# Kernel tuning notes

Measured on AMD Instinct MI355X. Metric: run time of the kernel, lower is better.

The kernel has to match this reference:

```python
import jax, jax.numpy as jnp
import numpy as np

B, N, K, H, HEADS = 4, 2000, 30, 128, 4
D = H // HEADS  # per-head dim = 32
NUM_IN = 2 * H
NEG_INF = jnp.float32(np.finfo(np.float32).min)


def setup_inputs() -> dict:
    key = jax.random.key(0)
    ks = jax.random.split(key, 10)
    h_V = jax.random.normal(ks[0], (B, N, H), jnp.float32)
    h_EV = jax.random.normal(ks[1], (B, N, K, NUM_IN), jnp.float32)
    h_KV = jax.random.normal(ks[2], (B, N, K, H), jnp.float32)
    h_KE = jax.random.normal(ks[3], (B, N, K, H), jnp.float32)
    mask_attend = (jax.random.uniform(ks[4], (B, N, K)) > 0.2).astype(jnp.float32)
    s = 1.0 / np.sqrt(H)
    W_Q = jax.random.normal(ks[5], (H, H), jnp.float32) * s
    W_K1 = jax.random.normal(ks[6], (H, H), jnp.float32) * s
    W_K2 = jax.random.normal(ks[7], (H, H), jnp.float32) * s
    W_V = jax.random.normal(ks[8], (H, NUM_IN), jnp.float32) * (1.0 / np.sqrt(NUM_IN))
    W_O = jax.random.normal(ks[9], (H, H), jnp.float32) * s
    return {"h_V": h_V, "h_EV": h_EV, "h_KV": h_KV, "h_KE": h_KE,
            "mask_attend": mask_attend, "W_Q": W_Q, "W_K1": W_K1,
            "W_K2": W_K2, "W_V": W_V, "W_O": W_O}


def reference(h_V, h_EV, h_KV, h_KE, mask_attend, W_Q, W_K1, W_K2, W_V, W_O):
    # Projections (torch Linear: y = x @ W.T)
    Q = (h_V @ W_Q.T).reshape(B, N, 1, HEADS, D)          # broadcast over K
    K1 = (h_KE @ W_K1.T).reshape(B, N, K, HEADS, D)
    K2 = (h_KV @ W_K2.T).reshape(B, N, K, HEADS, D)
    V = (h_EV @ W_V.T).reshape(B, N, K, HEADS, D)
    # Trilinear score: sum_d Q*K1*K2 -> [B,N,K,h] -> [B,N,h,K], scaled by 1/d
    logits = jnp.einsum('bnkhd,bnkhd->bnkh', Q * K1, K2)
    logits = jnp.transpose(logits, (0, 1, 3, 2)) / D      # [B,N,h,K]
    # Masked softmax over neighbor axis
    mask = jnp.broadcast_to(mask_attend[:, :, None, :], logits.shape)
    logits = jnp.where(mask > 0, logits, NEG_INF)
    attend = jax.nn.softmax(logits, axis=-1) * mask       # [B,N,h,K]
    # Weighted aggregation over neighbors
    h_upd = jnp.einsum('bnhk,bnkhd->bnhd', attend, V).reshape(B, N, H)
    return h_upd @ W_O.T
```

## Files before the change

kernel.cpp:

```cpp
#include <hip/hip_runtime.h>


#define KNB 30
#define HH 128
#define NUMIN 256
#define TOK 8000
#define TOTROW (TOK*KNB)
#define TB 2
#define NBLK (TOK/TB)
#define SAW 136

typedef __bf16 bf16x8 __attribute__((ext_vector_type(8)));
typedef __bf16 bf16x4_t __attribute__((ext_vector_type(4)));
typedef float f32x4 __attribute__((ext_vector_type(4)));

__global__ __launch_bounds__(256) void conv_w_kernel(
    const float* __restrict__ wk1, const float* __restrict__ wk2,
    const float* __restrict__ wv, __bf16* __restrict__ ws) {
  int e = (blockIdx.x * 256 + threadIdx.x) * 4;
  const float* src; int off;
  if (e < 16384)      { src = wk1; off = e; }
  else if (e < 32768) { src = wk2; off = e - 16384; }
  else                { src = wv;  off = e - 32768; }
  float4 v = *(const float4*)(src + off);
  bf16x4_t o4;
  o4.x = (__bf16)v.x; o4.y = (__bf16)v.y; o4.z = (__bf16)v.z; o4.w = (__bf16)v.w;
  *(bf16x4_t*)(ws + e) = o4;
}

__global__ __launch_bounds__(256, 4) void na_main_kernel(
    const float* __restrict__ h_V, const float* __restrict__ h_EV,
    const float* __restrict__ h_KV, const float* __restrict__ h_KE,
    const float* __restrict__ maskp, const float* __restrict__ W_Q,
    const float* __restrict__ W_O, const __bf16* __restrict__ bW,
    float* __restrict__ out) {
  __shared__ __bf16 sA[2][64 * SAW];
  __shared__ float sQ[TB][HH];
  __shared__ float sU[TB][HH];
  __shared__ float sMask[TB][32];

  const int tid = threadIdx.x;
  const int lane = tid & 63;
  const int wave = tid >> 6;
  const int m = lane & 15;
  const int quad = lane >> 4;
  const int t0 = blockIdx.x * TB;

  const __bf16* bWK1 = bW;
  const __bf16* bWK2 = bW + 16384;
  const __bf16* bWV  = bW + 32768;

  const int srow = tid >> 5;
  const int scol = (tid & 31) << 2;
  float4 sv[8];
  const long r0 = (long)t0 * KNB + srow;

  auto stage_load = [&](const float* base, int ld, int coloff) {
#pragma unroll
    for (int j = 0; j < 8; j++) {
      long rr = r0 + j * 8;
      if (rr > TOTROW - 1) rr = TOTROW - 1;
      sv[j] = *(const float4*)(base + rr * ld + coloff + scol);
    }
  };
  auto stage_store = [&](int b) {
#pragma unroll
    for (int j = 0; j < 8; j++) {
      bf16x4_t o;
      o.x = (__bf16)sv[j].x; o.y = (__bf16)sv[j].y;
      o.z = (__bf16)sv[j].z; o.w = (__bf16)sv[j].w;
      *(bf16x4_t*)&sA[b][(srow + j * 8) * SAW + scol] = o;
    }
  };

  f32x4 accA[4][2], accB[4][2];
  const f32x4 fzero = {0.f, 0.f, 0.f, 0.f};
  auto gemm = [&](const __bf16* gW, int ldw, int kb, const __bf16* Ab,
                  f32x4 (*acc)[2]) {
#pragma unroll
    for (int ks = 0; ks < 4; ks++) {
      const int kc = kb + ks * 32 + quad * 8;
      bf16x8 b0 = *(const bf16x8*)(gW + (wave * 32 + m) * ldw + kc);
      bf16x8 b1 = *(const bf16x8*)(gW + (wave * 32 + 16 + m) * ldw + kc);
#pragma unroll
      for (int mt = 0; mt < 4; mt++) {
        bf16x8 a = *(const bf16x8*)&Ab[(mt * 16 + m) * SAW + ks * 32 + quad * 8];
        acc[mt][0] = __builtin_amdgcn_mfma_f32_16x16x32_bf16(a, b0, acc[mt][0], 0, 0, 0);
        acc[mt][1] = __builtin_amdgcn_mfma_f32_16x16x32_bf16(a, b1, acc[mt][1], 0, 0, 0);
      }
    }
  };

  stage_load(h_KE, HH, 0);
  if (tid < TB * KNB)
    sMask[tid / KNB][tid % KNB] = maskp[(long)t0 * KNB + tid];
  {
    const int t = tid >> 7, o = tid & 127;
    const float4* wq = (const float4*)(W_Q + o * HH);
    const float4* hv = (const float4*)(h_V + (long)(t0 + t) * HH);
    float acc = 0.f;
#pragma unroll
    for (int j = 0; j < 32; j++) {
      float4 a = hv[j], b = wq[j];
      acc += a.x * b.x + a.y * b.y + a.z * b.z + a.w * b.w;
    }
    sQ[t][o] = acc;
  }
  stage_store(0);
  __syncthreads();

  stage_load(h_KV, HH, 0);
#pragma unroll
  for (int mt = 0; mt < 4; mt++) { accA[mt][0] = fzero; accA[mt][1] = fzero; }
  gemm(bWK1, HH, 0, sA[0], accA);
  stage_store(1);
  __syncthreads();

#pragma unroll
  for (int mt = 0; mt < 4; mt++) { accB[mt][0] = fzero; accB[mt][1] = fzero; }
  gemm(bWK2, HH, 0, sA[1], accB);
#pragma unroll
  for (int mt = 0; mt < 4; mt++) {
    accA[mt][0] *= accB[mt][0];
    accA[mt][1] *= accB[mt][1];
  }

  stage_load(h_EV, NUMIN, 0);

  float q0[2], q1[2];
#pragma unroll
  for (int nt = 0; nt < 2; nt++) {
    q0[nt] = sQ[0][wave * 32 + nt * 16 + m];
    q1[nt] = sQ[1][wave * 32 + nt * 16 + m];
  }
  float lg[4][4];
#pragma unroll
  for (int mt = 0; mt < 4; mt++)
#pragma unroll
    for (int r = 0; r < 4; r++) {
      int R = mt * 16 + quad * 4 + r;
      float qa0 = (R < 30) ? q0[0] : q1[0];
      float qa1 = (R < 30) ? q0[1] : q1[1];
      lg[mt][r] = accA[mt][0][r] * qa0 + accA[mt][1][r] * qa1;
    }
#pragma unroll
  for (int d = 1; d < 16; d <<= 1)
#pragma unroll
    for (int mt = 0; mt < 4; mt++)
#pragma unroll
      for (int r = 0; r < 4; r++)
        lg[mt][r] += __shfl_xor(lg[mt][r], d);

  float mx0 = -3.0e38f, mx1 = -3.0e38f;
#pragma unroll
  for (int mt = 0; mt < 4; mt++)
#pragma unroll
    for (int r = 0; r < 4; r++) {
      int R = mt * 16 + quad * 4 + r;
      if (R < 60) {
        int t = R >= 30, k = R - 30 * t;
        float l = (sMask[t][k] > 0.f) ? lg[mt][r] * 0.03125f : -3.0e38f;
        lg[mt][r] = l;
        if (t == 0) mx0 = fmaxf(mx0, l); else mx1 = fmaxf(mx1, l);
      } else lg[mt][r] = -3.0e38f;
    }
  mx0 = fmaxf(mx0, __shfl_xor(mx0, 16)); mx0 = fmaxf(mx0, __shfl_xor(mx0, 32));
  mx1 = fmaxf(mx1, __shfl_xor(mx1, 16)); mx1 = fmaxf(mx1, __shfl_xor(mx1, 32));
  float s0 = 0.f, s1 = 0.f;
  float at[4][4];
#pragma unroll
  for (int mt = 0; mt < 4; mt++)
#pragma unroll
    for (int r = 0; r < 4; r++) {
      int R = mt * 16 + quad * 4 + r;
      float e = 0.f;
      if (R < 60) {
        int t = R >= 30, k = R - 30 * t;
        if (sMask[t][k] > 0.f) {
          float mxt = (t == 0) ? mx0 : mx1;
          e = __expf(lg[mt][r] - mxt);
        }
        if (t == 0) s0 += e; else s1 += e;
      }
      at[mt][r] = e;
    }
  s0 += __shfl_xor(s0, 16); s0 += __shfl_xor(s0, 32);
  s1 += __shfl_xor(s1, 16); s1 += __shfl_xor(s1, 32);
  float inv0 = (s0 > 0.f) ? 1.f / s0 : 0.f;
  float inv1 = (s1 > 0.f) ? 1.f / s1 : 0.f;
#pragma unroll
  for (int mt = 0; mt < 4; mt++)
#pragma unroll
    for (int r = 0; r < 4; r++) {
      int R = mt * 16 + quad * 4 + r;
      at[mt][r] *= (R < 30) ? inv0 : inv1;
    }

  stage_store(0);
  __syncthreads();

  stage_load(h_EV, NUMIN, 128);
#pragma unroll
  for (int mt = 0; mt < 4; mt++) { accB[mt][0] = fzero; accB[mt][1] = fzero; }
  gemm(bWV, NUMIN, 0, sA[0], accB);
  stage_store(1);
  __syncthreads();

  gemm(bWV, NUMIN, 128, sA[1], accB);

  float u00 = 0.f, u01 = 0.f, u10 = 0.f, u11 = 0.f;
#pragma unroll
  for (int mt = 0; mt < 4; mt++)
#pragma unroll
    for (int r = 0; r < 4; r++) {
      int R = mt * 16 + quad * 4 + r;
      if (R < 30) {
        u00 += at[mt][r] * accB[mt][0][r];
        u01 += at[mt][r] * accB[mt][1][r];
      } else if (R < 60) {
        u10 += at[mt][r] * accB[mt][0][r];
        u11 += at[mt][r] * accB[mt][1][r];
      }
    }
  u00 += __shfl_xor(u00, 16); u00 += __shfl_xor(u00, 32);
  u01 += __shfl_xor(u01, 16); u01 += __shfl_xor(u01, 32);
  u10 += __shfl_xor(u10, 16); u10 += __shfl_xor(u10, 32);
  u11 += __shfl_xor(u11, 16); u11 += __shfl_xor(u11, 32);
  if (quad == 0) {
    sU[0][wave * 32 + m]      = u00;
    sU[0][wave * 32 + 16 + m] = u01;
    sU[1][wave * 32 + m]      = u10;
    sU[1][wave * 32 + 16 + m] = u11;
  }
  __syncthreads();

  {
    const int t = tid >> 7, o = tid & 127;
    const float4* wo = (const float4*)(W_O + o * HH);
    const float4* u = (const float4*)&sU[t][0];
    float r = 0.f;
#pragma unroll
    for (int j = 0; j < 32; j++) {
      float4 a = u[j], b = wo[j];
      r += a.x * b.x + a.y * b.y + a.z * b.z + a.w * b.w;
    }
    out[(long)(t0 + t) * HH + o] = r;
  }
}

extern "C" void kernel_launch(void* const* d_in, const int* in_sizes, int n_in,
                              void* d_out, int out_size, void* d_ws, size_t ws_size,
                              hipStream_t stream) {
  const float* h_V  = (const float*)d_in[0];
  const float* h_EV = (const float*)d_in[1];
  const float* h_KV = (const float*)d_in[2];
  const float* h_KE = (const float*)d_in[3];
  const float* mask = (const float*)d_in[4];
  const float* W_Q  = (const float*)d_in[5];
  const float* W_K1 = (const float*)d_in[6];
  const float* W_K2 = (const float*)d_in[7];
  const float* W_V  = (const float*)d_in[8];
  const float* W_O  = (const float*)d_in[9];
  __bf16* bW = (__bf16*)d_ws;

  conv_w_kernel<<<64, 256, 0, stream>>>(W_K1, W_K2, W_V, bW);
  na_main_kernel<<<NBLK, 256, 0, stream>>>(h_V, h_EV, h_KV, h_KE, mask,
                                           W_Q, W_O, bW, (float*)d_out);
}
```

Before: 629.0 us.

## Loop over four token tiles per block with double-buffered register prefetch

Each block now handles 8 tokens as 4 sequential 2-token tiles instead of 2 tokens. The next tile's KE/KV loads are prefetched into a second register buffer while the current tile's GEMMs run, and the W_Q/W_O projections are amortized over 4 tokens per thread to cut redundant weight reads. This doubles the staging registers and lowers the launch-bounds occupancy hint from 4 to 3 blocks, and it launches a quarter as many blocks.

```diff
diff --git a/kernel.cpp b/kernel.cpp
--- a/kernel.cpp
+++ b/kernel.cpp
@@ -6,8 +6,9 @@
 #define NUMIN 256
 #define TOK 8000
 #define TOTROW (TOK*KNB)
-#define TB 2
-#define NBLK (TOK/TB)
+#define TILES 4
+#define TOKB (2*TILES)
+#define NBLK (TOK/TOKB)
 #define SAW 136
 
 typedef __bf16 bf16x8 __attribute__((ext_vector_type(8)));
@@ -28,23 +29,23 @@
   *(bf16x4_t*)(ws + e) = o4;
 }
 
-__global__ __launch_bounds__(256, 4) void na_main_kernel(
+__global__ __launch_bounds__(256, 3) void na_main_kernel(
     const float* __restrict__ h_V, const float* __restrict__ h_EV,
     const float* __restrict__ h_KV, const float* __restrict__ h_KE,
     const float* __restrict__ maskp, const float* __restrict__ W_Q,
     const float* __restrict__ W_O, const __bf16* __restrict__ bW,
     float* __restrict__ out) {
   __shared__ __bf16 sA[2][64 * SAW];
-  __shared__ float sQ[TB][HH];
-  __shared__ float sU[TB][HH];
-  __shared__ float sMask[TB][32];
+  __shared__ float sQ[TOKB][HH];
+  __shared__ float sU[TOKB][HH];
+  __shared__ float sMask[TOKB][32];
 
   const int tid = threadIdx.x;
   const int lane = tid & 63;
   const int wave = tid >> 6;
   const int m = lane & 15;
   const int quad = lane >> 4;
-  const int t0 = blockIdx.x * TB;
+  const int tok0 = blockIdx.x * TOKB;
 
   const __bf16* bWK1 = bW;
   const __bf16* bWK2 = bW + 16384;
@@ -52,18 +53,20 @@
 
   const int srow = tid >> 5;
   const int scol = (tid & 31) << 2;
-  float4 sv[8];
-  const long r0 = (long)t0 * KNB + srow;
-
-  auto stage_load = [&](const float* base, int ld, int coloff) {
+
+  float4 svA[8], svB[8];
+
+  auto stage_load = [&](float4 (&sv)[8], const float* base, int ld, int tile,
+                        int coloff) {
+    const long r0 = (long)(tok0 + 2 * tile) * KNB + srow;
 #pragma unroll
     for (int j = 0; j < 8; j++) {
       long rr = r0 + j * 8;
       if (rr > TOTROW - 1) rr = TOTROW - 1;
-      sv[j] = *(const float4*)(base + rr * ld + coloff + scol);
+      sv[j] = *(const float4*)(base + rr * (long)ld + coloff + scol);
     }
   };
-  auto stage_store = [&](int b) {
+  auto stage_store = [&](float4 (&sv)[8], int b) {
 #pragma unroll
     for (int j = 0; j < 8; j++) {
       bf16x4_t o;
@@ -91,160 +94,175 @@
     }
   };
 
-  stage_load(h_KE, HH, 0);
-  if (tid < TB * KNB)
-    sMask[tid / KNB][tid % KNB] = maskp[(long)t0 * KNB + tid];
+  stage_load(svB, h_KE, HH, 0, 0);
+  stage_load(svA, h_KV, HH, 0, 0);
+  if (tid < TOKB * KNB)
+    sMask[tid / KNB][tid % KNB] = maskp[(long)tok0 * KNB + tid];
   {
-    const int t = tid >> 7, o = tid & 127;
+    const int o = tid & 127, g = tid >> 7;
     const float4* wq = (const float4*)(W_Q + o * HH);
-    const float4* hv = (const float4*)(h_V + (long)(t0 + t) * HH);
-    float acc = 0.f;
+    float qa[4] = {0.f, 0.f, 0.f, 0.f};
 #pragma unroll
     for (int j = 0; j < 32; j++) {
-      float4 a = hv[j], b = wq[j];
-      acc += a.x * b.x + a.y * b.y + a.z * b.z + a.w * b.w;
-    }
-    sQ[t][o] = acc;
+      float4 b = wq[j];
+#pragma unroll
+      for (int t = 0; t < 4; t++) {
+        float4 a = *(const float4*)(h_V + (long)(tok0 + g * 4 + t) * HH + j * 4);
+        qa[t] += a.x * b.x + a.y * b.y + a.z * b.z + a.w * b.w;
+      }
+    }
+#pragma unroll
+    for (int t = 0; t < 4; t++) sQ[g * 4 + t][o] = qa[t];
   }
-  stage_store(0);
+  stage_store(svB, 0);
   __syncthreads();
 
-  stage_load(h_KV, HH, 0);
-#pragma unroll
-  for (int mt = 0; mt < 4; mt++) { accA[mt][0] = fzero; accA[mt][1] = fzero; }
-  gemm(bWK1, HH, 0, sA[0], accA);
-  stage_store(1);
-  __syncthreads();
-
-#pragma unroll
-  for (int mt = 0; mt < 4; mt++) { accB[mt][0] = fzero; accB[mt][1] = fzero; }
-  gemm(bWK2, HH, 0, sA[1], accB);
-#pragma unroll
-  for (int mt = 0; mt < 4; mt++) {
-    accA[mt][0] *= accB[mt][0];
-    accA[mt][1] *= accB[mt][1];
+  for (int it = 0; it < TILES; ++it) {
+    const int tb = 2 * it;
+    float lg[4][4];
+
+    stage_load(svB, h_EV, NUMIN, it, 0);
+#pragma unroll
+    for (int mt = 0; mt < 4; mt++) { accA[mt][0] = fzero; accA[mt][1] = fzero; }
+    gemm(bWK1, HH, 0, sA[0], accA);
+    stage_store(svA, 1);
+    __syncthreads();
+
+    stage_load(svA, h_EV, NUMIN, it, 128);
+#pragma unroll
+    for (int mt = 0; mt < 4; mt++) { accB[mt][0] = fzero; accB[mt][1] = fzero; }
+    gemm(bWK2, HH, 0, sA[1], accB);
+#pragma unroll
+    for (int mt = 0; mt < 4; mt++) {
+      accA[mt][0] *= accB[mt][0];
+      accA[mt][1] *= accB[mt][1];
+    }
+    {
+      float q0[2], q1[2];
+#pragma unroll
+      for (int nt = 0; nt < 2; nt++) {
+        q0[nt] = sQ[tb][wave * 32 + nt * 16 + m];
+        q1[nt] = sQ[tb + 1][wave * 32 + nt * 16 + m];
+      }
+#pragma unroll
+      for (int mt = 0; mt < 4; mt++)
+#pragma unroll
+        for (int r = 0; r < 4; r++) {
+          int R = mt * 16 + quad * 4 + r;
+          float qa0 = (R < 30) ? q0[0] : q1[0];
+          float qa1 = (R < 30) ? q0[1] : q1[1];
+          lg[mt][r] = accA[mt][0][r] * qa0 + accA[mt][1][r] * qa1;
+        }
+#pragma unroll
+      for (int d = 1; d < 16; d <<= 1)
+#pragma unroll
+        for (int mt = 0; mt < 4; mt++)
+#pragma unroll
+          for (int r = 0; r < 4; r++)
+            lg[mt][r] += __shfl_xor(lg[mt][r], d);
+
+      float mx0 = -3.0e38f, mx1 = -3.0e38f;
+#pragma unroll
+      for (int mt = 0; mt < 4; mt++)
+#pragma unroll
+        for (int r = 0; r < 4; r++) {
+          int R = mt * 16 + quad * 4 + r;
+          if (R < 60) {
+            int t = R >= 30, k = R - 30 * t;
+            float l = (sMask[tb + t][k] > 0.f) ? lg[mt][r] * 0.03125f : -3.0e38f;
+            lg[mt][r] = l;
+            if (t == 0) mx0 = fmaxf(mx0, l); else mx1 = fmaxf(mx1, l);
+          } else lg[mt][r] = -3.0e38f;
+        }
+      mx0 = fmaxf(mx0, __shfl_xor(mx0, 16)); mx0 = fmaxf(mx0, __shfl_xor(mx0, 32));
+      mx1 = fmaxf(mx1, __shfl_xor(mx1, 16)); mx1 = fmaxf(mx1, __shfl_xor(mx1, 32));
+      float s0 = 0.f, s1 = 0.f;
+#pragma unroll
+      for (int mt = 0; mt < 4; mt++)
+#pragma unroll
+        for (int r = 0; r < 4; r++) {
+          int R = mt * 16 + quad * 4 + r;
+          float e = 0.f;
+          if (R < 60) {
+            int t = R >= 30, k = R - 30 * t;
+            if (sMask[tb + t][k] > 0.f) {
+              float mxt = (t == 0) ? mx0 : mx1;
+              e = __expf(lg[mt][r] - mxt);
+            }
+            if (t == 0) s0 += e; else s1 += e;
+          }
+          lg[mt][r] = e;
+        }
+      s0 += __shfl_xor(s0, 16); s0 += __shfl_xor(s0, 32);
+      s1 += __shfl_xor(s1, 16); s1 += __shfl_xor(s1, 32);
+      float inv0 = (s0 > 0.f) ? 1.f / s0 : 0.f;
+      float inv1 = (s1 > 0.f) ? 1.f / s1 : 0.f;
+#pragma unroll
+      for (int mt = 0; mt < 4; mt++)
+#pragma unroll
+        for (int r = 0; r < 4; r++) {
+          int R = mt * 16 + quad * 4 + r;
+          lg[mt][r] *= (R < 30) ? inv0 : inv1;
+        }
+    }
+    stage_store(svB, 0);
+    __syncthreads();
+
+    if (it + 1 < TILES) stage_load(svB, h_KE, HH, it + 1, 0);
+#pragma unroll
+    for (int mt = 0; mt < 4; mt++) { accB[mt][0] = fzero; accB[mt][1] = fzero; }
+    gemm(bWV, NUMIN, 0, sA[0], accB);
+    stage_store(svA, 1);
+    __syncthreads();
+
+    if (it + 1 < TILES) stage_load(svA, h_KV, HH, it + 1, 0);
+    gemm(bWV, NUMIN, 128, sA[1], accB);
+    {
+      float u00 = 0.f, u01 = 0.f, u10 = 0.f, u11 = 0.f;
+#pragma unroll
+      for (int mt = 0; mt < 4; mt++)
+#pragma unroll
+        for (int r = 0; r < 4; r++) {
+          int R = mt * 16 + quad * 4 + r;
+          if (R < 30) {
+            u00 += lg[mt][r] * accB[mt][0][r];
+            u01 += lg[mt][r] * accB[mt][1][r];
+          } else if (R < 60) {
+            u10 += lg[mt][r] * accB[mt][0][r];
+            u11 += lg[mt][r] * accB[mt][1][r];
+          }
+        }
+      u00 += __shfl_xor(u00, 16); u00 += __shfl_xor(u00, 32);
+      u01 += __shfl_xor(u01, 16); u01 += __shfl_xor(u01, 32);
+      u10 += __shfl_xor(u10, 16); u10 += __shfl_xor(u10, 32);
+      u11 += __shfl_xor(u11, 16); u11 += __shfl_xor(u11, 32);
+      if (quad == 0) {
+        sU[tb][wave * 32 + m]          = u00;
+        sU[tb][wave * 32 + 16 + m]     = u01;
+        sU[tb + 1][wave * 32 + m]      = u10;
+        sU[tb + 1][wave * 32 + 16 + m] = u11;
+      }
+    }
+    if (it + 1 < TILES) stage_store(svB, 0);
+    __syncthreads();
   }
 
-  stage_load(h_EV, NUMIN, 0);
-
-  float q0[2], q1[2];
-#pragma unroll
-  for (int nt = 0; nt < 2; nt++) {
-    q0[nt] = sQ[0][wave * 32 + nt * 16 + m];
-    q1[nt] = sQ[1][wave * 32 + nt * 16 + m];
-  }
-  float lg[4][4];
-#pragma unroll
-  for (int mt = 0; mt < 4; mt++)
-#pragma unroll
-    for (int r = 0; r < 4; r++) {
-      int R = mt * 16 + quad * 4 + r;
-      float qa0 = (R < 30) ? q0[0] : q1[0];
-      float qa1 = (R < 30) ? q0[1] : q1[1];
-      lg[mt][r] = accA[mt][0][r] * qa0 + accA[mt][1][r] * qa1;
-    }
-#pragma unroll
-  for (int d = 1; d < 16; d <<= 1)
-#pragma unroll
-    for (int mt = 0; mt < 4; mt++)
-#pragma unroll
-      for (int r = 0; r < 4; r++)
-        lg[mt][r] += __shfl_xor(lg[mt][r], d);
-
-  float mx0 = -3.0e38f, mx1 = -3.0e38f;
-#pragma unroll
-  for (int mt = 0; mt < 4; mt++)
-#pragma unroll
-    for (int r = 0; r < 4; r++) {
-      int R = mt * 16 + quad * 4 + r;
-      if (R < 60) {
-        int t = R >= 30, k = R - 30 * t;
-        float l = (sMask[t][k] > 0.f) ? lg[mt][r] * 0.03125f : -3.0e38f;
-        lg[mt][r] = l;
-        if (t == 0) mx0 = fmaxf(mx0, l); else mx1 = fmaxf(mx1, l);
-      } else lg[mt][r] = -3.0e38f;
-    }
-  mx0 = fmaxf(mx0, __shfl_xor(mx0, 16)); mx0 = fmaxf(mx0, __shfl_xor(mx0, 32));
-  mx1 = fmaxf(mx1, __shfl_xor(mx1, 16)); mx1 = fmaxf(mx1, __shfl_xor(mx1, 32));
-  float s0 = 0.f, s1 = 0.f;
-  float at[4][4];
-#pragma unroll
-  for (int mt = 0; mt < 4; mt++)
-#pragma unroll
-    for (int r = 0; r < 4; r++) {
-      int R = mt * 16 + quad * 4 + r;
-      float e = 0.f;
-      if (R < 60) {
-        int t = R >= 30, k = R - 30 * t;
-        if (sMask[t][k] > 0.f) {
-          float mxt = (t == 0) ? mx0 : mx1;
-          e = __expf(lg[mt][r] - mxt);
-        }
-        if (t == 0) s0 += e; else s1 += e;
-      }
-      at[mt][r] = e;
-    }
-  s0 += __shfl_xor(s0, 16); s0 += __shfl_xor(s0, 32);
-  s1 += __shfl_xor(s1, 16); s1 += __shfl_xor(s1, 32);
-  float inv0 = (s0 > 0.f) ? 1.f / s0 : 0.f;
-  float inv1 = (s1 > 0.f) ? 1.f / s1 : 0.f;
-#pragma unroll
-  for (int mt = 0; mt < 4; mt++)
-#pragma unroll
-    for (int r = 0; r < 4; r++) {
-      int R = mt * 16 + quad * 4 + r;
-      at[mt][r] *= (R < 30) ? inv0 : inv1;
-    }
-
-  stage_store(0);
-  __syncthreads();
-
-  stage_load(h_EV, NUMIN, 128);
-#pragma unroll
-  for (int mt = 0; mt < 4; mt++) { accB[mt][0] = fzero; accB[mt][1] = fzero; }
-  gemm(bWV, NUMIN, 0, sA[0], accB);
-  stage_store(1);
-  __syncthreads();
-
-  gemm(bWV, NUMIN, 128, sA[1], accB);
-
-  float u00 = 0.f, u01 = 0.f, u10 = 0.f, u11 = 0.f;
-#pragma unroll
-  for (int mt = 0; mt < 4; mt++)
-#pragma unroll
-    for (int r = 0; r < 4; r++) {
-      int R = mt * 16 + quad * 4 + r;
-      if (R < 30) {
-        u00 += at[mt][r] * accB[mt][0][r];
-        u01 += at[mt][r] * accB[mt][1][r];
-      } else if (R < 60) {
-        u10 += at[mt][r] * accB[mt][0][r];
-        u11 += at[mt][r] * accB[mt][1][r];
-      }
-    }
-  u00 += __shfl_xor(u00, 16); u00 += __shfl_xor(u00, 32);
-  u01 += __shfl_xor(u01, 16); u01 += __shfl_xor(u01, 32);
-  u10 += __shfl_xor(u10, 16); u10 += __shfl_xor(u10, 32);
-  u11 += __shfl_xor(u11, 16); u11 += __shfl_xor(u11, 32);
-  if (quad == 0) {
-    sU[0][wave * 32 + m]      = u00;
-    sU[0][wave * 32 + 16 + m] = u01;
-    sU[1][wave * 32 + m]      = u10;
-    sU[1][wave * 32 + 16 + m] = u11;
-  }
-  __syncthreads();
-
   {
-    const int t = tid >> 7, o = tid & 127;
+    const int o = tid & 127, g = tid >> 7;
     const float4* wo = (const float4*)(W_O + o * HH);
-    const float4* u = (const float4*)&sU[t][0];
-    float r = 0.f;
+    float r[4] = {0.f, 0.f, 0.f, 0.f};
 #pragma unroll
     for (int j = 0; j < 32; j++) {
-      float4 a = u[j], b = wo[j];
-      r += a.x * b.x + a.y * b.y + a.z * b.z + a.w * b.w;
-    }
-    out[(long)(t0 + t) * HH + o] = r;
+      float4 b = wo[j];
+#pragma unroll
+      for (int t = 0; t < 4; t++) {
+        float4 a = *(const float4*)(&sU[g * 4 + t][j * 4]);
+        r[t] += a.x * b.x + a.y * b.y + a.z * b.z + a.w * b.w;
+      }
+    }
+#pragma unroll
+    for (int t = 0; t < 4; t++)
+      out[(long)(tok0 + g * 4 + t) * HH + o] = r[t];
   }
 }
 
```

Result: no change. 619.5 us (-1.5%).
